# Kernel tuning notes

Hardware: AMD Instinct MI355X
Metric: run time of the kernel (lower is better)

The kernel has to match this reference:

```python
import jax, jax.numpy as jnp
import numpy as np

D, NH, NL, NP, DFF = 256, 8, 4, 4, 1024
HD = D // NH
SHAPES = np.array([[100, 152], [50, 76], [25, 38], [13, 19]], dtype=np.int64)
LV = int((SHAPES[:, 0] * SHAPES[:, 1]).sum())  # 20197


def setup_inputs() -> dict:
    key = jax.random.key(0)
    ks = iter(jax.random.split(key, 48))
    bs, Lq = 8, 300

    def w(shape, s=0.02):
        return jax.random.normal(next(ks), shape, jnp.float32) * s

    lsi = np.concatenate([[0], np.cumsum(SHAPES[:, 0] * SHAPES[:, 1])[:-1]]).astype(np.int64)
    return dict(
        tgt=w((bs, Lq, D), 1.0),
        query_pos=w((bs, Lq, D), 1.0),
        reference_points=jax.random.uniform(next(ks), (bs, Lq, NL, 2), jnp.float32),
        src=w((bs, LV, D), 1.0),
        in_proj_w=w((3 * D, D)), in_proj_b=jnp.zeros((3 * D,), jnp.float32),
        out_proj_w=w((D, D)), out_proj_b=jnp.zeros((D,), jnp.float32),
        samp_off_w=w((NH * NL * NP * 2, D)), samp_off_b=w((NH * NL * NP * 2,), 0.5),
        attn_w_w=w((NH * NL * NP, D)), attn_w_b=jnp.zeros((NH * NL * NP,), jnp.float32),
        value_proj_w=w((D, D)), value_proj_b=jnp.zeros((D,), jnp.float32),
        output_proj_w=w((D, D)), output_proj_b=jnp.zeros((D,), jnp.float32),
        lin1_w=w((DFF, D)), lin1_b=jnp.zeros((DFF,), jnp.float32),
        lin2_w=w((D, DFF)), lin2_b=jnp.zeros((D,), jnp.float32),
        norm1_w=jnp.ones((D,), jnp.float32), norm1_b=jnp.zeros((D,), jnp.float32),
        norm2_w=jnp.ones((D,), jnp.float32), norm2_b=jnp.zeros((D,), jnp.float32),
        norm3_w=jnp.ones((D,), jnp.float32), norm3_b=jnp.zeros((D,), jnp.float32),
        spatial_shapes=SHAPES,            # static numpy (shapes must be static)
        level_start_index=lsi,            # static numpy
        padding_mask=jnp.zeros((bs, LV), bool),
    )


def _ln(x, w, b):
    m = x.mean(-1, keepdims=True)
    v = ((x - m) ** 2).mean(-1, keepdims=True)
    return (x - m) * jax.lax.rsqrt(v + 1e-5) * w + b


def _bilinear(vflat, H_, W_, loc):
    # vflat: (b,h,H*W,d); loc: (b,h,q,p,2) normalized to [0,1]
    # matches F.grid_sample(align_corners=False, padding_mode='zeros')
    x = loc[..., 0] * W_ - 0.5
    y = loc[..., 1] * H_ - 0.5
    x0f, y0f = jnp.floor(x), jnp.floor(y)
    lx, ly = x - x0f, y - y0f
    x0, y0 = x0f.astype(jnp.int32), y0f.astype(jnp.int32)
    b, h, q, p = x0.shape

    def gather(ix, iy, wgt):
        valid = (ix >= 0) & (ix < W_) & (iy >= 0) & (iy < H_)
        idx = (jnp.clip(iy, 0, H_ - 1) * W_ + jnp.clip(ix, 0, W_ - 1)).reshape(b, h, q * p)
        g = jnp.take_along_axis(vflat, idx[..., None], axis=2)  # (b,h,q*p,d)
        return g * (wgt * valid).reshape(b, h, q * p, 1)

    out = (gather(x0, y0, (1 - lx) * (1 - ly)) + gather(x0 + 1, y0, lx * (1 - ly))
           + gather(x0, y0 + 1, (1 - lx) * ly) + gather(x0 + 1, y0 + 1, lx * ly))
    return out.reshape(b, h, q, p, -1)


def reference(tgt, query_pos, reference_points, src, in_proj_w, in_proj_b,
              out_proj_w, out_proj_b, samp_off_w, samp_off_b, attn_w_w, attn_w_b,
              value_proj_w, value_proj_b, output_proj_w, output_proj_b,
              lin1_w, lin1_b, lin2_w, lin2_b, norm1_w, norm1_b, norm2_w, norm2_b,
              norm3_w, norm3_b, spatial_shapes, level_start_index, padding_mask):
    bs, Lq, _ = tgt.shape
    ss = np.asarray(spatial_shapes)
    lsi = np.asarray(level_start_index)

    # ---- self attention (eval mode, dropout off) ----
    qk = tgt + query_pos
    qh = (qk @ in_proj_w[:D].T + in_proj_b[:D]).reshape(bs, Lq, NH, HD)
    kh = (qk @ in_proj_w[D:2 * D].T + in_proj_b[D:2 * D]).reshape(bs, Lq, NH, HD)
    vh = (tgt @ in_proj_w[2 * D:].T + in_proj_b[2 * D:]).reshape(bs, Lq, NH, HD)
    scores = jnp.einsum('bqhd,bkhd->bhqk', qh, kh) / jnp.sqrt(jnp.float32(HD))
    attn = jax.nn.softmax(scores, axis=-1)
    sa = jnp.einsum('bhqk,bkhd->bqhd', attn, vh).reshape(bs, Lq, D)
    sa = sa @ out_proj_w.T + out_proj_b
    x = _ln(tgt + sa, norm2_w, norm2_b)

    # ---- MSDeformAttn cross attention ----
    query = x + query_pos
    value = src @ value_proj_w.T + value_proj_b
    value = jnp.where(padding_mask[..., None], 0.0, value)
    value_t = value.reshape(bs, -1, NH, HD).transpose(0, 2, 1, 3)  # (b,h,Lv,d)

    offsets = (query @ samp_off_w.T + samp_off_b).reshape(bs, Lq, NH, NL, NP, 2)
    aw = jax.nn.softmax((query @ attn_w_w.T + attn_w_b).reshape(bs, Lq, NH, NL * NP), -1)
    aw = aw.reshape(bs, Lq, NH, NL, NP)
    norma = jnp.asarray(np.stack([ss[:, 1], ss[:, 0]], -1), jnp.float32)  # (NL,2)=[W,H]
    loc = reference_points[:, :, None, :, None, :] + offsets / norma[None, None, None, :, None, :]

    out = jnp.zeros((bs, Lq, NH, HD), value.dtype)
    for l in range(NL):
        H_, W_ = int(ss[l, 0]), int(ss[l, 1])
        s0 = int(lsi[l])
        vl = value_t[:, :, s0:s0 + H_ * W_]                    # (b,h,HW,d)
        ll = loc[:, :, :, l].transpose(0, 2, 1, 3, 4)          # (b,h,q,p,2)
        samp = _bilinear(vl, H_, W_, ll)                       # (b,h,q,p,d)
        out = out + jnp.einsum('bhqpd,bqhp->bqhd', samp, aw[:, :, :, l])
    ca = out.reshape(bs, Lq, D) @ output_proj_w.T + output_proj_b
    x = _ln(x + ca, norm1_w, norm1_b)

    # ---- FFN ----
    ffn = jax.nn.relu(x @ lin1_w.T + lin1_b) @ lin2_w.T + lin2_b
    x = _ln(x + ffn, norm3_w, norm3_b)
    return (x, loc, aw)
```

## Files before the change

kernel.cpp:

```cpp
#include <hip/hip_runtime.h>
#include <hip/hip_bf16.h>

#define D_ 256
#define NH_ 8
#define HD_ 32
#define NL_ 4
#define NP_ 4
#define DFF_ 1024
#define BS_ 8
#define LQ_ 300
#define LV_ 20197
#define NQ_ (BS_*LQ_)
#define MPAD_ 2432
#define NSRC_ (BS_*LV_*D_)

typedef short bf16x8 __attribute__((ext_vector_type(8)));
typedef float f32x4  __attribute__((ext_vector_type(4)));

__device__ __forceinline__ float u2f(unsigned int u) {
    union { unsigned int i; float f; } v; v.i = u << 16; return v.f;
}
__device__ __forceinline__ float lo2f(unsigned int u) {
    union { unsigned int i; float f; } v; v.i = u << 16; return v.f;
}
__device__ __forceinline__ float hi2f(unsigned int u) {
    union { unsigned int i; float f; } v; v.i = u & 0xffff0000u; return v.f;
}
__device__ __forceinline__ unsigned short f2bf_bits(float f) {
    __hip_bfloat16 b = __float2bfloat16(f);
    union { __hip_bfloat16 b; unsigned short u; } v; v.b = b; return v.u;
}
__device__ __forceinline__ ushort4 cv4(float4 a) {
    ushort4 o; o.x=f2bf_bits(a.x); o.y=f2bf_bits(a.y); o.z=f2bf_bits(a.z); o.w=f2bf_bits(a.w);
    return o;
}

__global__ __launch_bounds__(256) void cvt_bf16_kernel(
    const float* __restrict__ src, unsigned short* __restrict__ vbf)
{
    const int nsrc4 = NSRC_/4;
    for (int i = blockIdx.x*256 + threadIdx.x; i < nsrc4; i += gridDim.x*256) {
        ((ushort4*)vbf)[i] = cv4(((const float4*)src)[i]);
    }
}

__global__ __launch_bounds__(256) void cvt_misc_kernel(
    const float4* __restrict__ tgt, const float4* __restrict__ qp,
    const float4* __restrict__ ipw, const float4* __restrict__ l1w,
    const float4* __restrict__ l2w, const float4* __restrict__ opw,
    const float4* __restrict__ outw, const float4* __restrict__ sow,
    const float4* __restrict__ aww,
    ushort4* __restrict__ tgt_bf, ushort4* __restrict__ qk_bf,
    ushort4* __restrict__ ipw_bf, ushort4* __restrict__ l1w_bf,
    ushort4* __restrict__ l2w_bf, ushort4* __restrict__ opw_bf,
    ushort4* __restrict__ outw_bf, ushort4* __restrict__ sow_bf,
    ushort4* __restrict__ aww_bf)
{
    const int i = blockIdx.x*256 + threadIdx.x;
    if (i < 153600) {
        float4 a = tgt[i], b = qp[i];
        tgt_bf[i] = cv4(a);
        qk_bf[i]  = cv4(make_float4(a.x+b.x, a.y+b.y, a.z+b.z, a.w+b.w));
    } else if (i < 202752) { int j = i - 153600; ipw_bf[j]  = cv4(ipw[j]);
    } else if (i < 268288) { int j = i - 202752; l1w_bf[j]  = cv4(l1w[j]);
    } else if (i < 333824) { int j = i - 268288; l2w_bf[j]  = cv4(l2w[j]);
    } else if (i < 350208) { int j = i - 333824; opw_bf[j]  = cv4(opw[j]);
    } else if (i < 366592) { int j = i - 350208; outw_bf[j] = cv4(outw[j]);
    } else if (i < 382976) { int j = i - 366592; sow_bf[j]  = cv4(sow[j]);
    } else if (i < 391168) { int j = i - 382976; aww_bf[j]  = cv4(aww[j]);
    }
}

__global__ __launch_bounds__(256) void pack_vpw_kernel(
    const float4* __restrict__ vpw, float4* __restrict__ vpwP)
{
    __shared__ float4 tile[32][33];
    const int by = blockIdx.x >> 1, bx = blockIdx.x & 1;
    const int tx = threadIdx.x & 31, ty = threadIdx.x >> 5;
#pragma unroll
    for (int i = 0; i < 32; i += 8)
        tile[ty+i][tx] = vpw[(size_t)(by*32+ty+i)*64 + bx*32+tx];
    __syncthreads();
#pragma unroll
    for (int i = 0; i < 32; i += 8)
        vpwP[(size_t)(bx*32+ty+i)*256 + by*32+tx] = tile[tx][ty+i];
}

__global__ __launch_bounds__(256) void gemm_bf16_kernel(
    const unsigned short* __restrict__ A,
    const unsigned short* __restrict__ W,
    const float* __restrict__ bias,
    float* __restrict__ out,
    unsigned short* __restrict__ out_bf,
    const int K, const int Nld, const int relu)
{
    const int t = threadIdx.x, wv = t >> 6, l = t & 63;
    const int m_base = blockIdx.x*64 + wv*16;
    const int n_base = blockIdx.y*64;
    const int lr = l & 15, lg = l >> 4;
    const unsigned short* ap = A + (size_t)(m_base + lr)*K + lg*8;
    const unsigned short* wp = W + (size_t)(n_base + lr)*K + lg*8;
    f32x4 ac0 = {0,0,0,0}, ac1 = {0,0,0,0}, ac2 = {0,0,0,0}, ac3 = {0,0,0,0};
    for (int k = 0; k < K; k += 32) {
        bf16x8 a  = *(const bf16x8*)(ap + k);
        bf16x8 b0 = *(const bf16x8*)(wp + k);
        bf16x8 b1 = *(const bf16x8*)(wp + (size_t)16*K + k);
        bf16x8 b2 = *(const bf16x8*)(wp + (size_t)32*K + k);
        bf16x8 b3 = *(const bf16x8*)(wp + (size_t)48*K + k);
        ac0 = __builtin_amdgcn_mfma_f32_16x16x32_bf16(a, b0, ac0, 0, 0, 0);
        ac1 = __builtin_amdgcn_mfma_f32_16x16x32_bf16(a, b1, ac1, 0, 0, 0);
        ac2 = __builtin_amdgcn_mfma_f32_16x16x32_bf16(a, b2, ac2, 0, 0, 0);
        ac3 = __builtin_amdgcn_mfma_f32_16x16x32_bf16(a, b3, ac3, 0, 0, 0);
    }
    const int orow0 = m_base + lg*4;
    const int ocol  = n_base + lr;
    const float b0v = bias[ocol], b1v = bias[ocol+16],
                b2v = bias[ocol+32], b3v = bias[ocol+48];
#pragma unroll
    for (int j = 0; j < 4; ++j) {
        const int row = orow0 + j;
        if (row < NQ_) {
            float v0 = ac0[j] + b0v, v1 = ac1[j] + b1v,
                  v2 = ac2[j] + b2v, v3 = ac3[j] + b3v;
            if (relu) {
                v0 = fmaxf(v0, 0.f); v1 = fmaxf(v1, 0.f);
                v2 = fmaxf(v2, 0.f); v3 = fmaxf(v3, 0.f);
            }
            const size_t base = (size_t)row*Nld + ocol;
            if (out) {
                out[base]    = v0; out[base+16] = v1;
                out[base+32] = v2; out[base+48] = v3;
            }
            if (out_bf) {
                out_bf[base]    = f2bf_bits(v0); out_bf[base+16] = f2bf_bits(v1);
                out_bf[base+32] = f2bf_bits(v2); out_bf[base+48] = f2bf_bits(v3);
            }
        }
    }
}

__global__ __launch_bounds__(256) void attn_kernel(
    const float* __restrict__ qh, const float* __restrict__ kh,
    const float* __restrict__ vh, unsigned short* __restrict__ sa_bf)
{
    __shared__ unsigned short khl[LQ_][HD_+2];
    __shared__ unsigned short vhl[LQ_][HD_+2];
    __shared__ float sc[4][LQ_];
    __shared__ float qbuf[4][HD_];
    const int b = blockIdx.x >> 3, h = blockIdx.x & 7, chunk = blockIdx.y;
    const int t = threadIdx.x, w = t >> 6, lane = t & 63;
    for (int i = t; i < LQ_*HD_; i += 256) {
        int kq = i >> 5, d = i & 31;
        khl[kq][d] = f2bf_bits(kh[(b*LQ_ + kq)*D_ + h*HD_ + d]);
        vhl[kq][d] = f2bf_bits(vh[(b*LQ_ + kq)*D_ + h*HD_ + d]);
    }
    __syncthreads();
    const float scale = 0.17677669529663687f;
    for (int qi = 0; qi < 15; ++qi) {
        const int q = chunk*60 + w*15 + qi;
        if (lane < HD_) qbuf[w][lane] = qh[(b*LQ_ + q)*D_ + h*HD_ + lane];
        float qv[HD_];
#pragma unroll
        for (int d2 = 0; d2 < HD_; ++d2) qv[d2] = qbuf[w][d2];
        float mx = -1e30f;
        for (int k = lane; k < LQ_; k += 64) {
            float s = 0.f;
#pragma unroll
            for (int d2 = 0; d2 < HD_; ++d2) s += qv[d2]*u2f(khl[k][d2]);
            s *= scale;
            sc[w][k] = s;
            mx = fmaxf(mx, s);
        }
#pragma unroll
        for (int off = 32; off; off >>= 1) mx = fmaxf(mx, __shfl_xor(mx, off));
        float lsum = 0.f;
        for (int k = lane; k < LQ_; k += 64) {
            float e = __expf(sc[w][k] - mx);
            sc[w][k] = e; lsum += e;
        }
#pragma unroll
        for (int off = 32; off; off >>= 1) lsum += __shfl_xor(lsum, off);
        const int d = lane & 31, half = lane >> 5;
        float acc = 0.f;
        for (int k = half*150; k < half*150 + 150; ++k) acc += sc[w][k]*u2f(vhl[k][d]);
        acc += __shfl_down(acc, 32);
        if (lane < 32) sa_bf[(size_t)(b*LQ_ + q)*D_ + h*HD_ + d] = f2bf_bits(acc / lsum);
    }
}

__global__ __launch_bounds__(256) void res_ln_kernel(
    const float* __restrict__ y, const float* __restrict__ res,
    const float* __restrict__ gw, const float* __restrict__ gb,
    float* __restrict__ out, const float* __restrict__ qp,
    unsigned short* __restrict__ outq_bf, unsigned short* __restrict__ out_bf)
{
    __shared__ float2 part[4][8];
    const int t = threadIdx.x, m0 = blockIdx.x * 8;
    const int w = t >> 6, lane = t & 63;
    const float gwv = gw[t], gbv = gb[t];
    float v[8];
#pragma unroll
    for (int r = 0; r < 8; ++r) {
        v[r] = y[(m0+r)*D_+t] + res[(m0+r)*D_+t];
        float s = v[r], ss = v[r]*v[r];
#pragma unroll
        for (int off = 32; off; off >>= 1) {
            s += __shfl_xor(s, off); ss += __shfl_xor(ss, off);
        }
        if (lane == 0) part[w][r] = make_float2(s, ss);
    }
    __syncthreads();
#pragma unroll
    for (int r = 0; r < 8; ++r) {
        float2 p0 = part[0][r], p1 = part[1][r], p2 = part[2][r], p3 = part[3][r];
        float mean = (p0.x+p1.x+p2.x+p3.x) * (1.0f/256.0f);
        float ex2  = (p0.y+p1.y+p2.y+p3.y) * (1.0f/256.0f);
        float var  = ex2 - mean*mean;
        float o = (v[r]-mean) * rsqrtf(var + 1e-5f) * gwv + gbv;
        out[(m0+r)*D_+t] = o;
        if (outq_bf) outq_bf[(m0+r)*D_+t] = f2bf_bits(o + qp[(m0+r)*D_+t]);
        if (out_bf)  out_bf[(m0+r)*D_+t]  = f2bf_bits(o);
    }
}

__global__ __launch_bounds__(256) void samp_epi_kernel(
    const float* __restrict__ so, const float* __restrict__ awl,
    const float* __restrict__ refp,
    float* __restrict__ loc_out, float* __restrict__ aw_out)
{
    __shared__ float lg[8][128];
    const int t = threadIdx.x, m0 = blockIdx.x * 8;
    for (int i = t; i < 8*128; i += 256) lg[i >> 7][i & 127] = awl[m0*128 + i];
    __syncthreads();
    const int c_ = t & 1, l_ = (t >> 3) & 3;
    float nrm;
    if (c_ == 0) nrm = (l_==0)?152.f:(l_==1)?76.f:(l_==2)?38.f:19.f;
    else         nrm = (l_==0)?100.f:(l_==1)?50.f:(l_==2)?25.f:13.f;
#pragma unroll
    for (int r = 0; r < 8; ++r) {
        const int m = m0 + r;
        loc_out[m*256 + t] = refp[(m*NL_ + l_)*2 + c_] + so[m*256 + t] / nrm;
    }
    if (t < 128) {
        const int g0 = (t >> 4) << 4;
        for (int r = 0; r < 8; ++r) {
            float mx = -1e30f;
            for (int j = 0; j < 16; ++j) mx = fmaxf(mx, lg[r][g0+j]);
            float s = 0.f;
            for (int j = 0; j < 16; ++j) s += __expf(lg[r][g0+j] - mx);
            aw_out[(m0+r)*128 + t] = __expf(lg[r][t] - mx) / s;
        }
    }
}

__global__ __launch_bounds__(256) void samp_fuse_bf16_kernel(
    const unsigned short* __restrict__ vbf,
    const float* __restrict__ loc_f, const float* __restrict__ aw_f,
    float* __restrict__ svec_g, float* __restrict__ wsum_g)
{
    __shared__ int   cidx[128][4];
    __shared__ float cwt[128][4];
    const int m = blockIdx.x, t = threadIdx.x;
    const int b = m / LQ_;

    if (t < 128) {
        const int l = (t >> 2) & 3;
        const int HS[4] = {100,50,25,13}, WS[4] = {152,76,38,19}, S0[4] = {0,15200,19000,19950};
        const int Hh = HS[l], Ww = WS[l], s0 = S0[l];
        const float aw = aw_f[m*128 + t];
        const float x = loc_f[m*256 + 2*t]*Ww - 0.5f;
        const float y = loc_f[m*256 + 2*t + 1]*Hh - 0.5f;
        const float x0f = floorf(x), y0f = floorf(y);
        const int x0 = (int)x0f, y0 = (int)y0f;
        const float fx = x - x0f, fy = y - y0f;
        const int   cx[4] = {x0, x0+1, x0,   x0+1};
        const int   cy[4] = {y0, y0,   y0+1, y0+1};
        const float cw[4] = {(1.f-fx)*(1.f-fy), fx*(1.f-fy), (1.f-fx)*fy, fx*fy};
        float sw = 0.f;
#pragma unroll
        for (int j = 0; j < 4; ++j) {
            const bool valid = (cx[j] >= 0) & (cx[j] < Ww) & (cy[j] >= 0) & (cy[j] < Hh);
            cidx[t][j] = valid ? (s0 + cy[j]*Ww + cx[j]) : s0;
            float wv = valid ? aw*cw[j] : 0.f;
            cwt[t][j] = wv;
            sw += wv;
        }
#pragma unroll
        for (int off = 8; off; off >>= 1) sw += __shfl_xor(sw, off);
        if ((t & 15) == 0) wsum_g[m*NH_ + (t >> 4)] = sw;
    }
    __syncthreads();

    const int hh = (t >> 7) * 4;
    const int c  = t & 127;
    const unsigned int* sb = (const unsigned int*)(vbf + (size_t)b*LV_*D_) + c;
#pragma unroll
    for (int h = hh; h < hh + 4; ++h) {
        float e0=0.f, e1=0.f, e2=0.f, e3=0.f;
        float o0=0.f, o1=0.f, o2=0.f, o3=0.f;
#pragma unroll 4
        for (int s = 0; s < 16; ++s) {
            const int base = h*16 + s;
            const int   i0 = cidx[base][0], i1 = cidx[base][1],
                        i2 = cidx[base][2], i3 = cidx[base][3];
            const float w0 = cwt[base][0], w1 = cwt[base][1],
                        w2 = cwt[base][2], w3 = cwt[base][3];
            const unsigned int u0 = sb[(size_t)i0*128];
            const unsigned int u1 = sb[(size_t)i1*128];
            const unsigned int u2 = sb[(size_t)i2*128];
            const unsigned int u3 = sb[(size_t)i3*128];
            e0 += w0*lo2f(u0); o0 += w0*hi2f(u0);
            e1 += w1*lo2f(u1); o1 += w1*hi2f(u1);
            e2 += w2*lo2f(u2); o2 += w2*hi2f(u2);
            e3 += w3*lo2f(u3); o3 += w3*hi2f(u3);
        }
        *(float2*)&svec_g[(size_t)m*(NH_*D_) + h*D_ + 2*c] =
            make_float2((e0+e1)+(e2+e3), (o0+o1)+(o2+o3));
    }
}

__global__ __launch_bounds__(256) void vproj_kernel(
    const float* __restrict__ svec_g, const float* __restrict__ wsum_g,
    const float4* __restrict__ vpwP, const float* __restrict__ vpb,
    unsigned short* __restrict__ vo_bf)
{
    __shared__ float sv[4][NH_*D_];
    const int t = threadIdx.x, m0 = blockIdx.x * 4;
    for (int i = t; i < 4*NH_*D_; i += 256)
        sv[i >> 11][i & 2047] = svec_g[(size_t)m0*(NH_*D_) + i];
    __syncthreads();
    const int h = t >> 5;
    const float4* w4 = vpwP + t;
    float a0 = 0.f, a1 = 0.f, a2 = 0.f, a3 = 0.f;
    for (int c = 0; c < 64; ++c) {
        const float4 wq = w4[c*256];
        const float4 s0 = *(const float4*)&sv[0][h*D_ + c*4];
        const float4 s1 = *(const float4*)&sv[1][h*D_ + c*4];
        const float4 s2 = *(const float4*)&sv[2][h*D_ + c*4];
        const float4 s3 = *(const float4*)&sv[3][h*D_ + c*4];
        a0 += wq.x*s0.x + wq.y*s0.y + wq.z*s0.z + wq.w*s0.w;
        a1 += wq.x*s1.x + wq.y*s1.y + wq.z*s1.z + wq.w*s1.w;
        a2 += wq.x*s2.x + wq.y*s2.y + wq.z*s2.z + wq.w*s2.w;
        a3 += wq.x*s3.x + wq.y*s3.y + wq.z*s3.z + wq.w*s3.w;
    }
    const float bb = vpb[t];
    vo_bf[(size_t)(m0+0)*D_ + t] = f2bf_bits(a0 + bb*wsum_g[(m0+0)*NH_ + h]);
    vo_bf[(size_t)(m0+1)*D_ + t] = f2bf_bits(a1 + bb*wsum_g[(m0+1)*NH_ + h]);
    vo_bf[(size_t)(m0+2)*D_ + t] = f2bf_bits(a2 + bb*wsum_g[(m0+2)*NH_ + h]);
    vo_bf[(size_t)(m0+3)*D_ + t] = f2bf_bits(a3 + bb*wsum_g[(m0+3)*NH_ + h]);
}

extern "C" void kernel_launch(void* const* d_in, const int* in_sizes, int n_in,
                              void* d_out, int out_size, void* d_ws, size_t ws_size,
                              hipStream_t stream) {
    (void)in_sizes; (void)n_in; (void)out_size; (void)ws_size;
    const float* tgt  = (const float*)d_in[0];
    const float* qpos = (const float*)d_in[1];
    const float* refp = (const float*)d_in[2];
    const float* srcp = (const float*)d_in[3];
    const float* ipw  = (const float*)d_in[4];
    const float* ipb  = (const float*)d_in[5];
    const float* opw  = (const float*)d_in[6];
    const float* opb  = (const float*)d_in[7];
    const float* sow  = (const float*)d_in[8];
    const float* sob  = (const float*)d_in[9];
    const float* aww  = (const float*)d_in[10];
    const float* awb  = (const float*)d_in[11];
    const float* vpw  = (const float*)d_in[12];
    const float* vpb  = (const float*)d_in[13];
    const float* outw = (const float*)d_in[14];
    const float* outb = (const float*)d_in[15];
    const float* l1w  = (const float*)d_in[16];
    const float* l1b  = (const float*)d_in[17];
    const float* l2w  = (const float*)d_in[18];
    const float* l2b  = (const float*)d_in[19];
    const float* n1w  = (const float*)d_in[20];
    const float* n1b  = (const float*)d_in[21];
    const float* n2w  = (const float*)d_in[22];
    const float* n2b  = (const float*)d_in[23];
    const float* n3w  = (const float*)d_in[24];
    const float* n3b  = (const float*)d_in[25];

    float* wsf = (float*)d_ws;
    float* qh   = wsf;
    float* kh   = wsf + 614400;
    float* vh   = wsf + 1228800;
    float* x1   = wsf + 1843200;
    float* x2   = wsf + 2457600;
    float* y    = wsf + 3072000;
    float* so_o = wsf + 3686400;
    float* awl  = wsf + 4300800;
    unsigned short* hid_bf  = (unsigned short*)(wsf + 4608000);
    unsigned short* tgt_bf  = (unsigned short*)(wsf + 5853184);
    unsigned short* qk_bf   = (unsigned short*)(wsf + 6164480);
    unsigned short* sa_bf   = (unsigned short*)(wsf + 6475776);
    unsigned short* x1q_bf  = (unsigned short*)(wsf + 6787072);
    unsigned short* vo_bf   = (unsigned short*)(wsf + 7098368);
    unsigned short* x2_bf   = (unsigned short*)(wsf + 7409664);
    unsigned short* ipw_bf  = (unsigned short*)(wsf + 7720960);
    unsigned short* l1w_bf  = (unsigned short*)(wsf + 7819264);
    unsigned short* l2w_bf  = (unsigned short*)(wsf + 7950336);
    unsigned short* opw_bf  = (unsigned short*)(wsf + 8081408);
    unsigned short* outw_bf = (unsigned short*)(wsf + 8114176);
    unsigned short* sow_bf  = (unsigned short*)(wsf + 8146944);
    unsigned short* aww_bf  = (unsigned short*)(wsf + 8179712);
    float4* vpwP = (float4*)(wsf + 8196096);
    unsigned short* vbf = (unsigned short*)(wsf + 8261632);
    float* svec_g = wsf + 8261632 + 20681728;
    float* wsum_g = svec_g + 4915200;

    float* xout   = (float*)d_out;
    float* locout = xout + 614400;
    float* awout  = xout + 1228800;

    cvt_misc_kernel<<<1528, 256, 0, stream>>>(
        (const float4*)tgt, (const float4*)qpos, (const float4*)ipw,
        (const float4*)l1w, (const float4*)l2w, (const float4*)opw,
        (const float4*)outw, (const float4*)sow, (const float4*)aww,
        (ushort4*)tgt_bf, (ushort4*)qk_bf, (ushort4*)ipw_bf,
        (ushort4*)l1w_bf, (ushort4*)l2w_bf, (ushort4*)opw_bf,
        (ushort4*)outw_bf, (ushort4*)sow_bf, (ushort4*)aww_bf);
    pack_vpw_kernel<<<16, 256, 0, stream>>>((const float4*)vpw, vpwP);
    cvt_bf16_kernel<<<2048, 256, 0, stream>>>(srcp, vbf);

    gemm_bf16_kernel<<<dim3(38, 4), 256, 0, stream>>>(qk_bf,  ipw_bf,          ipb,       qh, nullptr, 256, 256, 0);
    gemm_bf16_kernel<<<dim3(38, 4), 256, 0, stream>>>(qk_bf,  ipw_bf + 65536,  ipb + 256, kh, nullptr, 256, 256, 0);
    gemm_bf16_kernel<<<dim3(38, 4), 256, 0, stream>>>(tgt_bf, ipw_bf + 131072, ipb + 512, vh, nullptr, 256, 256, 0);

    attn_kernel<<<dim3(BS_*NH_, 5), 256, 0, stream>>>(qh, kh, vh, sa_bf);

    gemm_bf16_kernel<<<dim3(38, 4), 256, 0, stream>>>(sa_bf, opw_bf, opb, y, nullptr, 256, 256, 0);
    res_ln_kernel<<<NQ_/8, 256, 0, stream>>>(y, tgt, n2w, n2b, x1, qpos, x1q_bf, nullptr);

    gemm_bf16_kernel<<<dim3(38, 4), 256, 0, stream>>>(x1q_bf, sow_bf, sob, so_o, nullptr, 256, 256, 0);
    gemm_bf16_kernel<<<dim3(38, 2), 256, 0, stream>>>(x1q_bf, aww_bf, awb, awl, nullptr, 256, 128, 0);
    samp_epi_kernel<<<NQ_/8, 256, 0, stream>>>(so_o, awl, refp, locout, awout);

    samp_fuse_bf16_kernel<<<NQ_, 256, 0, stream>>>(vbf, locout, awout, svec_g, wsum_g);
    vproj_kernel<<<NQ_/4, 256, 0, stream>>>(svec_g, wsum_g, vpwP, vpb, vo_bf);

    gemm_bf16_kernel<<<dim3(38, 4), 256, 0, stream>>>(vo_bf, outw_bf, outb, y, nullptr, 256, 256, 0);
    res_ln_kernel<<<NQ_/8, 256, 0, stream>>>(y, x1, n1w, n1b, x2, nullptr, nullptr, x2_bf);

    gemm_bf16_kernel<<<dim3(38, 16), 256, 0, stream>>>(x2_bf,  l1w_bf, l1b, nullptr, hid_bf, 256, 1024, 1);
    gemm_bf16_kernel<<<dim3(38, 4),  256, 0, stream>>>(hid_bf, l2w_bf, l2b, y, nullptr, 1024, 256, 0);
    res_ln_kernel<<<NQ_/8, 256, 0, stream>>>(y, x2, n3w, n3b, xout, nullptr, nullptr, nullptr);
}
```

Baseline: 550.9 us.

## Fuse conversions, QKV and offset GEMMs, GEMM+LayerNorm, and sampling epilogue

```diff
diff --git a/kernel.cpp b/kernel.cpp
--- a/kernel.cpp
+++ b/kernel.cpp
@@ -35,70 +35,77 @@
     return o;
 }
 
-__global__ __launch_bounds__(256) void cvt_bf16_kernel(
-    const float* __restrict__ src, unsigned short* __restrict__ vbf)
-{
-    const int nsrc4 = NSRC_/4;
-    for (int i = blockIdx.x*256 + threadIdx.x; i < nsrc4; i += gridDim.x*256) {
-        ((ushort4*)vbf)[i] = cv4(((const float4*)src)[i]);
-    }
-}
-
-__global__ __launch_bounds__(256) void cvt_misc_kernel(
-    const float4* __restrict__ tgt, const float4* __restrict__ qp,
-    const float4* __restrict__ ipw, const float4* __restrict__ l1w,
-    const float4* __restrict__ l2w, const float4* __restrict__ opw,
-    const float4* __restrict__ outw, const float4* __restrict__ sow,
-    const float4* __restrict__ aww,
-    ushort4* __restrict__ tgt_bf, ushort4* __restrict__ qk_bf,
-    ushort4* __restrict__ ipw_bf, ushort4* __restrict__ l1w_bf,
-    ushort4* __restrict__ l2w_bf, ushort4* __restrict__ opw_bf,
-    ushort4* __restrict__ outw_bf, ushort4* __restrict__ sow_bf,
-    ushort4* __restrict__ aww_bf)
-{
-    const int i = blockIdx.x*256 + threadIdx.x;
-    if (i < 153600) {
-        float4 a = tgt[i], b = qp[i];
-        tgt_bf[i] = cv4(a);
-        qk_bf[i]  = cv4(make_float4(a.x+b.x, a.y+b.y, a.z+b.z, a.w+b.w));
-    } else if (i < 202752) { int j = i - 153600; ipw_bf[j]  = cv4(ipw[j]);
-    } else if (i < 268288) { int j = i - 202752; l1w_bf[j]  = cv4(l1w[j]);
-    } else if (i < 333824) { int j = i - 268288; l2w_bf[j]  = cv4(l2w[j]);
-    } else if (i < 350208) { int j = i - 333824; opw_bf[j]  = cv4(opw[j]);
-    } else if (i < 366592) { int j = i - 350208; outw_bf[j] = cv4(outw[j]);
-    } else if (i < 382976) { int j = i - 366592; sow_bf[j]  = cv4(sow[j]);
-    } else if (i < 391168) { int j = i - 382976; aww_bf[j]  = cv4(aww[j]);
-    }
-}
-
-__global__ __launch_bounds__(256) void pack_vpw_kernel(
-    const float4* __restrict__ vpw, float4* __restrict__ vpwP)
+#define S0_ 10340864
+#define S1_ 10494464
+#define S2_ 10543616
+#define S3_ 10609152
+#define S4_ 10674688
+#define S5_ 10691072
+#define S6_ 10707456
+#define S7_ 10723840
+#define S8_ 10732032
+#define S9_ 10732128
+__global__ __launch_bounds__(256) void cvt_all_kernel(
+    const float4* __restrict__ src, const float4* __restrict__ tgt,
+    const float4* __restrict__ qp,  const float4* __restrict__ ipw,
+    const float4* __restrict__ l1w, const float4* __restrict__ l2w,
+    const float4* __restrict__ opw, const float4* __restrict__ outw,
+    const float4* __restrict__ sow, const float4* __restrict__ aww,
+    const float4* __restrict__ sob, const float4* __restrict__ awb,
+    const float4* __restrict__ vpw,
+    ushort4* __restrict__ vbf,    ushort4* __restrict__ tgt_bf,
+    ushort4* __restrict__ qk_bf,  ushort4* __restrict__ ipw_bf,
+    ushort4* __restrict__ l1w_bf, ushort4* __restrict__ l2w_bf,
+    ushort4* __restrict__ opw_bf, ushort4* __restrict__ outw_bf,
+    ushort4* __restrict__ sow_bf, ushort4* __restrict__ aww_bf,
+    float4* __restrict__ sawb,    float4* __restrict__ vpwP)
 {
     __shared__ float4 tile[32][33];
-    const int by = blockIdx.x >> 1, bx = blockIdx.x & 1;
-    const int tx = threadIdx.x & 31, ty = threadIdx.x >> 5;
-#pragma unroll
-    for (int i = 0; i < 32; i += 8)
-        tile[ty+i][tx] = vpw[(size_t)(by*32+ty+i)*64 + bx*32+tx];
-    __syncthreads();
-#pragma unroll
-    for (int i = 0; i < 32; i += 8)
-        vpwP[(size_t)(bx*32+ty+i)*256 + by*32+tx] = tile[tx][ty+i];
+    if (blockIdx.x < 16) {
+        const int by = blockIdx.x >> 1, bx = blockIdx.x & 1;
+        const int tx = threadIdx.x & 31, ty = threadIdx.x >> 5;
+#pragma unroll
+        for (int i = 0; i < 32; i += 8)
+            tile[ty+i][tx] = vpw[(size_t)(by*32+ty+i)*64 + bx*32+tx];
+        __syncthreads();
+#pragma unroll
+        for (int i = 0; i < 32; i += 8)
+            vpwP[(size_t)(bx*32+ty+i)*256 + by*32+tx] = tile[tx][ty+i];
+    }
+    for (int i = blockIdx.x*256 + threadIdx.x; i < S9_; i += 2048*256) {
+        if (i < S0_) { vbf[i] = cv4(src[i]); }
+        else if (i < S1_) {
+            int j = i - S0_;
+            float4 a = tgt[j], b = qp[j];
+            tgt_bf[j] = cv4(a);
+            qk_bf[j]  = cv4(make_float4(a.x+b.x, a.y+b.y, a.z+b.z, a.w+b.w));
+        }
+        else if (i < S2_) { int j = i - S1_; ipw_bf[j]  = cv4(ipw[j]); }
+        else if (i < S3_) { int j = i - S2_; l1w_bf[j]  = cv4(l1w[j]); }
+        else if (i < S4_) { int j = i - S3_; l2w_bf[j]  = cv4(l2w[j]); }
+        else if (i < S5_) { int j = i - S4_; opw_bf[j]  = cv4(opw[j]); }
+        else if (i < S6_) { int j = i - S5_; outw_bf[j] = cv4(outw[j]); }
+        else if (i < S7_) { int j = i - S6_; sow_bf[j]  = cv4(sow[j]); }
+        else if (i < S8_) { int j = i - S7_; aww_bf[j]  = cv4(aww[j]); }
+        else { int j = i - S8_; sawb[j] = (j < 64) ? sob[j] : awb[j-64]; }
+    }
 }
 
 __global__ __launch_bounds__(256) void gemm_bf16_kernel(
     const unsigned short* __restrict__ A,
+    const unsigned short* __restrict__ A2,
     const unsigned short* __restrict__ W,
     const float* __restrict__ bias,
     float* __restrict__ out,
     unsigned short* __restrict__ out_bf,
-    const int K, const int Nld, const int relu)
+    const int K, const int Nld, const int relu, const int nsplit)
 {
     const int t = threadIdx.x, wv = t >> 6, l = t & 63;
     const int m_base = blockIdx.x*64 + wv*16;
     const int n_base = blockIdx.y*64;
     const int lr = l & 15, lg = l >> 4;
-    const unsigned short* ap = A + (size_t)(m_base + lr)*K + lg*8;
+    const unsigned short* Au = (n_base < nsplit) ? A : A2;
+    const unsigned short* ap = Au + (size_t)(m_base + lr)*K + lg*8;
     const unsigned short* wp = W + (size_t)(n_base + lr)*K + lg*8;
     f32x4 ac0 = {0,0,0,0}, ac1 = {0,0,0,0}, ac2 = {0,0,0,0}, ac3 = {0,0,0,0};
     for (int k = 0; k < K; k += 32) {
@@ -139,9 +146,74 @@
     }
 }
 
+__global__ __launch_bounds__(256) void gemm_ln_kernel(
+    const unsigned short* __restrict__ A,
+    const unsigned short* __restrict__ W,
+    const float* __restrict__ bias, const float* __restrict__ res,
+    const float* __restrict__ gw, const float* __restrict__ gb,
+    float* __restrict__ out,
+    const float* __restrict__ qp,
+    unsigned short* __restrict__ outq_bf,
+    unsigned short* __restrict__ out_bf,
+    const int K)
+{
+    const int t = threadIdx.x, wv = t >> 6, l = t & 63;
+    const int m_base = blockIdx.x*64 + wv*16;
+    const int lr = l & 15, lg = l >> 4;
+    const unsigned short* ap = A + (size_t)(m_base + lr)*K + lg*8;
+    const unsigned short* wp = W + (size_t)lr*K + lg*8;
+    f32x4 acc[16];
+#pragma unroll
+    for (int nt = 0; nt < 16; ++nt) acc[nt] = (f32x4){0,0,0,0};
+    for (int k = 0; k < K; k += 32) {
+        bf16x8 a = *(const bf16x8*)(ap + k);
+#pragma unroll
+        for (int nt = 0; nt < 16; ++nt) {
+            bf16x8 b = *(const bf16x8*)(wp + (size_t)nt*16*K + k);
+            acc[nt] = __builtin_amdgcn_mfma_f32_16x16x32_bf16(a, b, acc[nt], 0, 0, 0);
+        }
+    }
+    float bl[16], gwl[16], gbl[16];
+#pragma unroll
+    for (int nt = 0; nt < 16; ++nt) {
+        const int col = nt*16 + lr;
+        bl[nt] = bias[col]; gwl[nt] = gw[col]; gbl[nt] = gb[col];
+    }
+#pragma unroll
+    for (int j = 0; j < 4; ++j) {
+        const int row = m_base + lg*4 + j;
+        const bool valid = row < NQ_;
+        float v[16];
+        float s = 0.f, ss = 0.f;
+#pragma unroll
+        for (int nt = 0; nt < 16; ++nt) {
+            float r = valid ? res[(size_t)row*256 + nt*16 + lr] : 0.f;
+            v[nt] = acc[nt][j] + bl[nt] + r;
+            s += v[nt]; ss += v[nt]*v[nt];
+        }
+#pragma unroll
+        for (int off = 1; off < 16; off <<= 1) {
+            s += __shfl_xor(s, off); ss += __shfl_xor(ss, off);
+        }
+        const float mean = s * (1.0f/256.0f);
+        const float var  = ss * (1.0f/256.0f) - mean*mean;
+        const float rs   = rsqrtf(var + 1e-5f);
+        if (valid) {
+#pragma unroll
+            for (int nt = 0; nt < 16; ++nt) {
+                const int col = nt*16 + lr;
+                const size_t idx = (size_t)row*256 + col;
+                const float o = (v[nt]-mean)*rs*gwl[nt] + gbl[nt];
+                out[idx] = o;
+                if (outq_bf) outq_bf[idx] = f2bf_bits(o + qp[idx]);
+                if (out_bf)  out_bf[idx]  = f2bf_bits(o);
+            }
+        }
+    }
+}
+
 __global__ __launch_bounds__(256) void attn_kernel(
-    const float* __restrict__ qh, const float* __restrict__ kh,
-    const float* __restrict__ vh, unsigned short* __restrict__ sa_bf)
+    const float* __restrict__ qkv, unsigned short* __restrict__ sa_bf)
 {
     __shared__ unsigned short khl[LQ_][HD_+2];
     __shared__ unsigned short vhl[LQ_][HD_+2];
@@ -151,14 +223,14 @@
     const int t = threadIdx.x, w = t >> 6, lane = t & 63;
     for (int i = t; i < LQ_*HD_; i += 256) {
         int kq = i >> 5, d = i & 31;
-        khl[kq][d] = f2bf_bits(kh[(b*LQ_ + kq)*D_ + h*HD_ + d]);
-        vhl[kq][d] = f2bf_bits(vh[(b*LQ_ + kq)*D_ + h*HD_ + d]);
+        khl[kq][d] = f2bf_bits(qkv[(size_t)(b*LQ_ + kq)*768 + 256 + h*HD_ + d]);
+        vhl[kq][d] = f2bf_bits(qkv[(size_t)(b*LQ_ + kq)*768 + 512 + h*HD_ + d]);
     }
     __syncthreads();
     const float scale = 0.17677669529663687f;
     for (int qi = 0; qi < 15; ++qi) {
         const int q = chunk*60 + w*15 + qi;
-        if (lane < HD_) qbuf[w][lane] = qh[(b*LQ_ + q)*D_ + h*HD_ + lane];
+        if (lane < HD_) qbuf[w][lane] = qkv[(size_t)(b*LQ_ + q)*768 + h*HD_ + lane];
         float qv[HD_];
 #pragma unroll
         for (int d2 = 0; d2 < HD_; ++d2) qv[d2] = qbuf[w][d2];
@@ -188,74 +260,10 @@
     }
 }
 
-__global__ __launch_bounds__(256) void res_ln_kernel(
-    const float* __restrict__ y, const float* __restrict__ res,
-    const float* __restrict__ gw, const float* __restrict__ gb,
-    float* __restrict__ out, const float* __restrict__ qp,
-    unsigned short* __restrict__ outq_bf, unsigned short* __restrict__ out_bf)
-{
-    __shared__ float2 part[4][8];
-    const int t = threadIdx.x, m0 = blockIdx.x * 8;
-    const int w = t >> 6, lane = t & 63;
-    const float gwv = gw[t], gbv = gb[t];
-    float v[8];
-#pragma unroll
-    for (int r = 0; r < 8; ++r) {
-        v[r] = y[(m0+r)*D_+t] + res[(m0+r)*D_+t];
-        float s = v[r], ss = v[r]*v[r];
-#pragma unroll
-        for (int off = 32; off; off >>= 1) {
-            s += __shfl_xor(s, off); ss += __shfl_xor(ss, off);
-        }
-        if (lane == 0) part[w][r] = make_float2(s, ss);
-    }
-    __syncthreads();
-#pragma unroll
-    for (int r = 0; r < 8; ++r) {
-        float2 p0 = part[0][r], p1 = part[1][r], p2 = part[2][r], p3 = part[3][r];
-        float mean = (p0.x+p1.x+p2.x+p3.x) * (1.0f/256.0f);
-        float ex2  = (p0.y+p1.y+p2.y+p3.y) * (1.0f/256.0f);
-        float var  = ex2 - mean*mean;
-        float o = (v[r]-mean) * rsqrtf(var + 1e-5f) * gwv + gbv;
-        out[(m0+r)*D_+t] = o;
-        if (outq_bf) outq_bf[(m0+r)*D_+t] = f2bf_bits(o + qp[(m0+r)*D_+t]);
-        if (out_bf)  out_bf[(m0+r)*D_+t]  = f2bf_bits(o);
-    }
-}
-
-__global__ __launch_bounds__(256) void samp_epi_kernel(
-    const float* __restrict__ so, const float* __restrict__ awl,
-    const float* __restrict__ refp,
-    float* __restrict__ loc_out, float* __restrict__ aw_out)
-{
-    __shared__ float lg[8][128];
-    const int t = threadIdx.x, m0 = blockIdx.x * 8;
-    for (int i = t; i < 8*128; i += 256) lg[i >> 7][i & 127] = awl[m0*128 + i];
-    __syncthreads();
-    const int c_ = t & 1, l_ = (t >> 3) & 3;
-    float nrm;
-    if (c_ == 0) nrm = (l_==0)?152.f:(l_==1)?76.f:(l_==2)?38.f:19.f;
-    else         nrm = (l_==0)?100.f:(l_==1)?50.f:(l_==2)?25.f:13.f;
-#pragma unroll
-    for (int r = 0; r < 8; ++r) {
-        const int m = m0 + r;
-        loc_out[m*256 + t] = refp[(m*NL_ + l_)*2 + c_] + so[m*256 + t] / nrm;
-    }
-    if (t < 128) {
-        const int g0 = (t >> 4) << 4;
-        for (int r = 0; r < 8; ++r) {
-            float mx = -1e30f;
-            for (int j = 0; j < 16; ++j) mx = fmaxf(mx, lg[r][g0+j]);
-            float s = 0.f;
-            for (int j = 0; j < 16; ++j) s += __expf(lg[r][g0+j] - mx);
-            aw_out[(m0+r)*128 + t] = __expf(lg[r][t] - mx) / s;
-        }
-    }
-}
-
 __global__ __launch_bounds__(256) void samp_fuse_bf16_kernel(
     const unsigned short* __restrict__ vbf,
-    const float* __restrict__ loc_f, const float* __restrict__ aw_f,
+    const float* __restrict__ so_awl, const float* __restrict__ refp,
+    float* __restrict__ locout, float* __restrict__ awout,
     float* __restrict__ svec_g, float* __restrict__ wsum_g)
 {
     __shared__ int   cidx[128][4];
@@ -267,9 +275,21 @@
         const int l = (t >> 2) & 3;
         const int HS[4] = {100,50,25,13}, WS[4] = {152,76,38,19}, S0[4] = {0,15200,19000,19950};
         const int Hh = HS[l], Ww = WS[l], s0 = S0[l];
-        const float aw = aw_f[m*128 + t];
-        const float x = loc_f[m*256 + 2*t]*Ww - 0.5f;
-        const float y = loc_f[m*256 + 2*t + 1]*Hh - 0.5f;
+        const float logit = so_awl[(size_t)m*384 + 256 + t];
+        float mx = logit;
+#pragma unroll
+        for (int off = 1; off < 16; off <<= 1) mx = fmaxf(mx, __shfl_xor(mx, off));
+        float e = __expf(logit - mx), esum = e;
+#pragma unroll
+        for (int off = 1; off < 16; off <<= 1) esum += __shfl_xor(esum, off);
+        const float aw = e / esum;
+        awout[(size_t)m*128 + t] = aw;
+        const float locx = refp[(m*NL_ + l)*2 + 0] + so_awl[(size_t)m*384 + 2*t]     / (float)Ww;
+        const float locy = refp[(m*NL_ + l)*2 + 1] + so_awl[(size_t)m*384 + 2*t + 1] / (float)Hh;
+        locout[(size_t)m*256 + 2*t]     = locx;
+        locout[(size_t)m*256 + 2*t + 1] = locy;
+        const float x = locx*Ww - 0.5f;
+        const float y = locy*Hh - 0.5f;
         const float x0f = floorf(x), y0f = floorf(y);
         const int x0 = (int)x0f, y0 = (int)y0f;
         const float fx = x - x0f, fy = y - y0f;
@@ -382,67 +402,64 @@
     const float* n3b  = (const float*)d_in[25];
 
     float* wsf = (float*)d_ws;
-    float* qh   = wsf;
-    float* kh   = wsf + 614400;
-    float* vh   = wsf + 1228800;
-    float* x1   = wsf + 1843200;
-    float* x2   = wsf + 2457600;
-    float* y    = wsf + 3072000;
-    float* so_o = wsf + 3686400;
-    float* awl  = wsf + 4300800;
-    unsigned short* hid_bf  = (unsigned short*)(wsf + 4608000);
-    unsigned short* tgt_bf  = (unsigned short*)(wsf + 5853184);
-    unsigned short* qk_bf   = (unsigned short*)(wsf + 6164480);
-    unsigned short* sa_bf   = (unsigned short*)(wsf + 6475776);
-    unsigned short* x1q_bf  = (unsigned short*)(wsf + 6787072);
-    unsigned short* vo_bf   = (unsigned short*)(wsf + 7098368);
-    unsigned short* x2_bf   = (unsigned short*)(wsf + 7409664);
-    unsigned short* ipw_bf  = (unsigned short*)(wsf + 7720960);
-    unsigned short* l1w_bf  = (unsigned short*)(wsf + 7819264);
-    unsigned short* l2w_bf  = (unsigned short*)(wsf + 7950336);
-    unsigned short* opw_bf  = (unsigned short*)(wsf + 8081408);
-    unsigned short* outw_bf = (unsigned short*)(wsf + 8114176);
-    unsigned short* sow_bf  = (unsigned short*)(wsf + 8146944);
-    unsigned short* aww_bf  = (unsigned short*)(wsf + 8179712);
-    float4* vpwP = (float4*)(wsf + 8196096);
-    unsigned short* vbf = (unsigned short*)(wsf + 8261632);
-    float* svec_g = wsf + 8261632 + 20681728;
+    float* qkv_buf = wsf;
+    float* x1      = wsf + 1843200;
+    float* x2      = wsf + 2457600;
+    float* so_awl  = wsf + 3072000;
+    unsigned short* hid_bf  = (unsigned short*)(wsf + 3993600);
+    unsigned short* tgt_bf  = (unsigned short*)(wsf + 5238784);
+    unsigned short* qk_bf   = (unsigned short*)(wsf + 5550080);
+    unsigned short* sa_bf   = (unsigned short*)(wsf + 5861376);
+    unsigned short* x1q_bf  = (unsigned short*)(wsf + 6172672);
+    unsigned short* vo_bf   = (unsigned short*)(wsf + 6483968);
+    unsigned short* x2_bf   = (unsigned short*)(wsf + 6795264);
+    unsigned short* ipw_bf  = (unsigned short*)(wsf + 7106560);
+    unsigned short* l1w_bf  = (unsigned short*)(wsf + 7204864);
+    unsigned short* l2w_bf  = (unsigned short*)(wsf + 7335936);
+    unsigned short* opw_bf  = (unsigned short*)(wsf + 7467008);
+    unsigned short* outw_bf = (unsigned short*)(wsf + 7499776);
+    unsigned short* sow_bf  = (unsigned short*)(wsf + 7532544);
+    unsigned short* aww_bf  = (unsigned short*)(wsf + 7565312);
+    float* sawb = wsf + 7581696;
+    float4* vpwP = (float4*)(wsf + 7582080);
+    unsigned short* vbf = (unsigned short*)(wsf + 7647616);
+    float* svec_g = wsf + 7647616 + 20681728;
     float* wsum_g = svec_g + 4915200;
 
     float* xout   = (float*)d_out;
     float* locout = xout + 614400;
     float* awout  = xout + 1228800;
 
-    cvt_misc_kernel<<<1528, 256, 0, stream>>>(
-        (const float4*)tgt, (const float4*)qpos, (const float4*)ipw,
-        (const float4*)l1w, (const float4*)l2w, (const float4*)opw,
-        (const float4*)outw, (const float4*)sow, (const float4*)aww,
-        (ushort4*)tgt_bf, (ushort4*)qk_bf, (ushort4*)ipw_bf,
-        (ushort4*)l1w_bf, (ushort4*)l2w_bf, (ushort4*)opw_bf,
-        (ushort4*)outw_bf, (ushort4*)sow_bf, (ushort4*)aww_bf);
-    pack_vpw_kernel<<<16, 256, 0, stream>>>((const float4*)vpw, vpwP);
-    cvt_bf16_kernel<<<2048, 256, 0, stream>>>(srcp, vbf);
-
-    gemm_bf16_kernel<<<dim3(38, 4), 256, 0, stream>>>(qk_bf,  ipw_bf,          ipb,       qh, nullptr, 256, 256, 0);
-    gemm_bf16_kernel<<<dim3(38, 4), 256, 0, stream>>>(qk_bf,  ipw_bf + 65536,  ipb + 256, kh, nullptr, 256, 256, 0);
-    gemm_bf16_kernel<<<dim3(38, 4), 256, 0, stream>>>(tgt_bf, ipw_bf + 131072, ipb + 512, vh, nullptr, 256, 256, 0);
-
-    attn_kernel<<<dim3(BS_*NH_, 5), 256, 0, stream>>>(qh, kh, vh, sa_bf);
-
-    gemm_bf16_kernel<<<dim3(38, 4), 256, 0, stream>>>(sa_bf, opw_bf, opb, y, nullptr, 256, 256, 0);
-    res_ln_kernel<<<NQ_/8, 256, 0, stream>>>(y, tgt, n2w, n2b, x1, qpos, x1q_bf, nullptr);
-
-    gemm_bf16_kernel<<<dim3(38, 4), 256, 0, stream>>>(x1q_bf, sow_bf, sob, so_o, nullptr, 256, 256, 0);
-    gemm_bf16_kernel<<<dim3(38, 2), 256, 0, stream>>>(x1q_bf, aww_bf, awb, awl, nullptr, 256, 128, 0);
-    samp_epi_kernel<<<NQ_/8, 256, 0, stream>>>(so_o, awl, refp, locout, awout);
-
-    samp_fuse_bf16_kernel<<<NQ_, 256, 0, stream>>>(vbf, locout, awout, svec_g, wsum_g);
+    cvt_all_kernel<<<2048, 256, 0, stream>>>(
+        (const float4*)srcp, (const float4*)tgt, (const float4*)qpos,
+        (const float4*)ipw, (const float4*)l1w, (const float4*)l2w,
+        (const float4*)opw, (const float4*)outw, (const float4*)sow,
+        (const float4*)aww, (const float4*)sob, (const float4*)awb,
+        (const float4*)vpw,
+        (ushort4*)vbf, (ushort4*)tgt_bf, (ushort4*)qk_bf, (ushort4*)ipw_bf,
+        (ushort4*)l1w_bf, (ushort4*)l2w_bf, (ushort4*)opw_bf, (ushort4*)outw_bf,
+        (ushort4*)sow_bf, (ushort4*)aww_bf, (float4*)sawb, vpwP);
+
+    gemm_bf16_kernel<<<dim3(38, 12), 256, 0, stream>>>(
+        qk_bf, tgt_bf, ipw_bf, ipb, qkv_buf, nullptr, 256, 768, 0, 512);
+
+    attn_kernel<<<dim3(BS_*NH_, 5), 256, 0, stream>>>(qkv_buf, sa_bf);
+
+    gemm_ln_kernel<<<38, 256, 0, stream>>>(sa_bf, opw_bf, opb, tgt, n2w, n2b,
+                                           x1, qpos, x1q_bf, nullptr, 256);
+
+    gemm_bf16_kernel<<<dim3(38, 6), 256, 0, stream>>>(
+        x1q_bf, x1q_bf, sow_bf, sawb, so_awl, nullptr, 256, 384, 0, 1<<30);
+
+    samp_fuse_bf16_kernel<<<NQ_, 256, 0, stream>>>(vbf, so_awl, refp,
+                                                   locout, awout, svec_g, wsum_g);
     vproj_kernel<<<NQ_/4, 256, 0, stream>>>(svec_g, wsum_g, vpwP, vpb, vo_bf);
 
-    gemm_bf16_kernel<<<dim3(38, 4), 256, 0, stream>>>(vo_bf, outw_bf, outb, y, nullptr, 256, 256, 0);
-    res_ln_kernel<<<NQ_/8, 256, 0, stream>>>(y, x1, n1w, n1b, x2, nullptr, nullptr, x2_bf);
-
-    gemm_bf16_kernel<<<dim3(38, 16), 256, 0, stream>>>(x2_bf,  l1w_bf, l1b, nullptr, hid_bf, 256, 1024, 1);
-    gemm_bf16_kernel<<<dim3(38, 4),  256, 0, stream>>>(hid_bf, l2w_bf, l2b, y, nullptr, 1024, 256, 0);
-    res_ln_kernel<<<NQ_/8, 256, 0, stream>>>(y, x2, n3w, n3b, xout, nullptr, nullptr, nullptr);
-}
+    gemm_ln_kernel<<<38, 256, 0, stream>>>(vo_bf, outw_bf, outb, x1, n1w, n1b,
+                                           x2, nullptr, nullptr, x2_bf, 256);
+
+    gemm_bf16_kernel<<<dim3(38, 16), 256, 0, stream>>>(
+        x2_bf, x2_bf, l1w_bf, l1b, nullptr, hid_bf, 256, 1024, 1, 1<<30);
+    gemm_ln_kernel<<<38, 256, 0, stream>>>(hid_bf, l2w_bf, l2b, x2, n3w, n3b,
+                                           xout, nullptr, nullptr, nullptr, 1024);
+}
```

New measurement: 676.3 us. 1.23x slower.
